# Optimization experiments

Measured on AMD Instinct MI355X. Metric: run time of the kernel, lower is better.

## Reference

```python
import jax, jax.numpy as jnp
import numpy as np

N, D, R, E = 50000, 128, 16, 1600000


def rgcn_conv(x, W, root, bias, src, dst, rel):
    """PyG-style RGCNConv (aggr='mean', root weight + bias).
    out[i] = x[i] @ root + bias + sum_r mean_{j in N_r(i)} x[j] @ W_r
    Aggregate-then-transform: segment-mean per (relation, dst) then contract with W.
    """
    n, d = x.shape
    seg = rel * n + dst  # combined (relation, dst-node) segment id
    msg_sum = jax.ops.segment_sum(x[src], seg, num_segments=R * n).reshape(R, n, d)
    cnt = jax.ops.segment_sum(jnp.ones_like(src, dtype=x.dtype), seg, num_segments=R * n).reshape(R, n, 1)
    msg = msg_sum / jnp.maximum(cnt, 1.0)  # mean aggregation (0 when no edges)
    return jnp.einsum('rnd,rde->ne', msg, W) + x @ root + bias


def setup_inputs() -> dict:
    key = jax.random.key(0)
    ks = jax.random.split(key, 9)
    x = jax.random.normal(ks[0], (N, D), dtype=jnp.float32)
    edge_index = jax.random.randint(ks[1], (2, E), 0, N, dtype=jnp.int64)
    edge_type = jax.random.randint(ks[2], (E,), 0, R, dtype=jnp.int64)
    s = 1.0 / np.sqrt(D)
    W1 = jax.random.normal(ks[3], (R, D, D), dtype=jnp.float32) * s
    root1 = jax.random.normal(ks[4], (D, D), dtype=jnp.float32) * s
    b1 = jnp.zeros((D,), dtype=jnp.float32)
    W2 = jax.random.normal(ks[5], (R, D, D), dtype=jnp.float32) * s
    root2 = jax.random.normal(ks[6], (D, D), dtype=jnp.float32) * s
    b2 = jnp.zeros((D,), dtype=jnp.float32)
    return {"x": x, "edge_index": edge_index, "edge_type": edge_type,
            "W1": W1, "root1": root1, "b1": b1,
            "W2": W2, "root2": root2, "b2": b2}


def reference(x, edge_index, edge_type, W1, root1, b1, W2, root2, b2):
    src, dst = edge_index[0], edge_index[1]
    # layer 1: RGCN -> ReLU -> Dropout (identity in eval mode)
    h = jax.nn.relu(rgcn_conv(x, W1, root1, b1, src, dst, edge_type))
    # layer 2: RGCN -> ReLU
    h = jax.nn.relu(rgcn_conv(h, W2, root2, b2, src, dst, edge_type))
    return h
```

## Files before the change

kernel.cpp:

```cpp
#include <hip/hip_runtime.h>


#define ND 128
#define NR 16
#define KPB 4096

typedef __attribute__((ext_vector_type(8))) short bf16x8;
typedef __attribute__((ext_vector_type(4))) float f32x4;

__device__ __forceinline__ unsigned short f2b(float f) {
    unsigned u = __float_as_uint(f);
    u += 0x7FFFu + ((u >> 16) & 1u);
    return (unsigned short)(u >> 16);
}

__global__ __launch_bounds__(256) void coarse_hist(
    const int* __restrict__ dst, const int* __restrict__ rel,
    int* __restrict__ coarse_cnt, int E, int N, int NBK)
{
    __shared__ int h[1024];
    const int t = threadIdx.x;
    for (int i = t; i < NBK; i += 256) h[i] = 0;
    __syncthreads();
#pragma unroll
    for (int q = 0; q < 16; ++q) {
        int e = blockIdx.x * KPB + q * 256 + t;
        if (e < E) {
            int key = rel[e] * N + dst[e];
            atomicAdd(&h[key >> 12], 1);
        }
    }
    __syncthreads();
    for (int i = t; i < NBK; i += 256)
        if (h[i]) atomicAdd(&coarse_cnt[i], h[i]);
}

__global__ __launch_bounds__(1024) void coarse_scan(
    const int* __restrict__ coarse_cnt, int* __restrict__ cscan,
    int* __restrict__ coarse_cursor, int NBK, int E)
{
    __shared__ int sdata[1024];
    const int t = threadIdx.x;
    int v = (t < NBK) ? coarse_cnt[t] : 0;
    sdata[t] = v;
    __syncthreads();
    for (int off = 1; off < 1024; off <<= 1) {
        int tmp = (t >= off) ? sdata[t - off] : 0;
        __syncthreads();
        sdata[t] += tmp;
        __syncthreads();
    }
    if (t < NBK) {
        int excl = sdata[t] - v;
        cscan[t] = excl;
        coarse_cursor[t] = excl;
    }
    if (t == 0) cscan[NBK] = E;
}

__global__ __launch_bounds__(256) void fillA(
    const int* __restrict__ src, const int* __restrict__ dst,
    const int* __restrict__ rel, int* __restrict__ coarse_cursor,
    uint2* __restrict__ coarse_buf, int E, int N, int NBK)
{
    __shared__ uint2 pairs[KPB];
    __shared__ int h[1024];
    const int t = threadIdx.x;
    for (int i = t; i < NBK; i += 256) h[i] = 0;
    __syncthreads();
#pragma unroll
    for (int q = 0; q < 16; ++q) {
        int e = blockIdx.x * KPB + q * 256 + t;
        unsigned key = 0xFFFFFFFFu, sv = 0;
        if (e < E) {
            key = (unsigned)(rel[e] * N + dst[e]);
            sv = (unsigned)src[e];
            atomicAdd(&h[key >> 12], 1);
        }
        pairs[q * 256 + t] = make_uint2(sv, key);
    }
    __syncthreads();
    for (int i = t; i < NBK; i += 256) {
        int c = h[i];
        h[i] = c ? atomicAdd(&coarse_cursor[i], c) : 0;
    }
    __syncthreads();
#pragma unroll
    for (int q = 0; q < 16; ++q) {
        uint2 p = pairs[q * 256 + t];
        if (p.y != 0xFFFFFFFFu) {
            int pos = atomicAdd(&h[p.y >> 12], 1);
            coarse_buf[pos] = p;
        }
    }
}

__global__ __launch_bounds__(256) void fillB(
    const uint2* __restrict__ coarse_buf, const int* __restrict__ cscan,
    int* __restrict__ seg_off, float* __restrict__ cnt_inv,
    int* __restrict__ sorted_src, int M, int E, int NBK)
{
    __shared__ int cnt[KPB];
    __shared__ int w[256];
    const int t = threadIdx.x;
    const int b = blockIdx.x;
    const int kbase = b << 12;
    const int nkeys = min(KPB, M - kbase);
    const int r0 = cscan[b], r1 = cscan[b + 1];

    for (int i = t; i < KPB; i += 256) cnt[i] = 0;
    __syncthreads();
    for (int e = r0 + t; e < r1; e += 256)
        atomicAdd(&cnt[coarse_buf[e].y - kbase], 1);
    __syncthreads();
    for (int i = t; i < nkeys; i += 256)
        cnt_inv[kbase + i] = 1.0f / fmaxf((float)cnt[i], 1.0f);
    int s = 0;
#pragma unroll
    for (int j = 0; j < 16; ++j) s += cnt[t * 16 + j];
    w[t] = s;
    __syncthreads();
    for (int off = 1; off < 256; off <<= 1) {
        int tmp = (t >= off) ? w[t - off] : 0;
        __syncthreads();
        w[t] += tmp;
        __syncthreads();
    }
    int run = r0 + w[t] - s;
#pragma unroll
    for (int j = 0; j < 16; ++j) {
        int i = t * 16 + j;
        int c = cnt[i];
        cnt[i] = run;
        if (i < nkeys) seg_off[kbase + i] = run;
        run += c;
    }
    if (b == NBK - 1 && t == 0) seg_off[M] = E;
    __syncthreads();
    for (int e = r0 + t; e < r1; e += 256) {
        uint2 p = coarse_buf[e];
        int pos = atomicAdd(&cnt[p.y - kbase], 1);
        sorted_src[pos] = (int)p.x;
    }
}

__global__ __launch_bounds__(256) void conv_x_kernel(
    const float* __restrict__ x, unsigned short* __restrict__ xb, int n4)
{
    int i = blockIdx.x * 256 + threadIdx.x;
    if (i >= n4) return;
    float4 v = ((const float4*)x)[i];
    uint2 o;
    o.x = (unsigned)f2b(v.x) | ((unsigned)f2b(v.y) << 16);
    o.y = (unsigned)f2b(v.z) | ((unsigned)f2b(v.w) << 16);
    ((uint2*)xb)[i] = o;
}

__global__ __launch_bounds__(256) void conv_w_kernel(
    const float* __restrict__ W, const float* __restrict__ root,
    unsigned short* __restrict__ Wt)
{
    int t = blockIdx.x * 256 + threadIdx.x;
    if (t >= 17 * 2048) return;
    int mat = t >> 11;
    int f = t & 2047;
    int lane = f & 63;
    int ctkt = f >> 6;
    int kt = ctkt >> 3;
    int ct = ctkt & 7;
    int n = ct * 16 + (lane & 15);
    int k = kt * 32 + (lane >> 4) * 8;
    const float* s = (mat < 16) ? (W + (size_t)mat * 16384) : root;
    uint4 o;
    o.x = (unsigned)f2b(s[(size_t)(k + 0) * ND + n]) | ((unsigned)f2b(s[(size_t)(k + 1) * ND + n]) << 16);
    o.y = (unsigned)f2b(s[(size_t)(k + 2) * ND + n]) | ((unsigned)f2b(s[(size_t)(k + 3) * ND + n]) << 16);
    o.z = (unsigned)f2b(s[(size_t)(k + 4) * ND + n]) | ((unsigned)f2b(s[(size_t)(k + 5) * ND + n]) << 16);
    o.w = (unsigned)f2b(s[(size_t)(k + 6) * ND + n]) | ((unsigned)f2b(s[(size_t)(k + 7) * ND + n]) << 16);
    *(uint4*)(Wt + (size_t)t * 8) = o;
}

__global__ __launch_bounds__(256) void gather_mean(
    const unsigned short* __restrict__ A,
    const int* __restrict__ seg_off,
    const int* __restrict__ sorted_src,
    const float* __restrict__ cnt_inv,
    unsigned short* __restrict__ msg,
    int N, int r0, int ccN)
{
    int g = blockIdx.x * 16 + (threadIdx.x >> 4);
    if (g >= ccN) return;
    int l = threadIdx.x & 15;
    int s = r0 * N + g;
    int b0 = seg_off[s], e1 = seg_off[s + 1];
    float a0 = 0.f, a1 = 0.f, a2 = 0.f, a3 = 0.f, a4 = 0.f, a5 = 0.f, a6 = 0.f, a7 = 0.f;
    int e = b0;
    for (; e + 2 <= e1; e += 2) {
        int s0 = sorted_src[e];
        int s1 = sorted_src[e + 1];
        uint4 u0 = *(const uint4*)(A + (size_t)s0 * ND + l * 8);
        uint4 u1 = *(const uint4*)(A + (size_t)s1 * ND + l * 8);
        a0 += __uint_as_float(u0.x << 16); a1 += __uint_as_float(u0.x & 0xFFFF0000u);
        a2 += __uint_as_float(u0.y << 16); a3 += __uint_as_float(u0.y & 0xFFFF0000u);
        a4 += __uint_as_float(u0.z << 16); a5 += __uint_as_float(u0.z & 0xFFFF0000u);
        a6 += __uint_as_float(u0.w << 16); a7 += __uint_as_float(u0.w & 0xFFFF0000u);
        a0 += __uint_as_float(u1.x << 16); a1 += __uint_as_float(u1.x & 0xFFFF0000u);
        a2 += __uint_as_float(u1.y << 16); a3 += __uint_as_float(u1.y & 0xFFFF0000u);
        a4 += __uint_as_float(u1.z << 16); a5 += __uint_as_float(u1.z & 0xFFFF0000u);
        a6 += __uint_as_float(u1.w << 16); a7 += __uint_as_float(u1.w & 0xFFFF0000u);
    }
    if (e < e1) {
        int s0 = sorted_src[e];
        uint4 u0 = *(const uint4*)(A + (size_t)s0 * ND + l * 8);
        a0 += __uint_as_float(u0.x << 16); a1 += __uint_as_float(u0.x & 0xFFFF0000u);
        a2 += __uint_as_float(u0.y << 16); a3 += __uint_as_float(u0.y & 0xFFFF0000u);
        a4 += __uint_as_float(u0.z << 16); a5 += __uint_as_float(u0.z & 0xFFFF0000u);
        a6 += __uint_as_float(u0.w << 16); a7 += __uint_as_float(u0.w & 0xFFFF0000u);
    }
    float inv = cnt_inv[s];
    uint4 o;
    o.x = (unsigned)f2b(a0 * inv) | ((unsigned)f2b(a1 * inv) << 16);
    o.y = (unsigned)f2b(a2 * inv) | ((unsigned)f2b(a3 * inv) << 16);
    o.z = (unsigned)f2b(a4 * inv) | ((unsigned)f2b(a5 * inv) << 16);
    o.w = (unsigned)f2b(a6 * inv) | ((unsigned)f2b(a7 * inv) << 16);
    *(uint4*)(msg + (size_t)g * ND + l * 8) = o;
}

__global__ __launch_bounds__(256) void gemm_mfma(
    const unsigned short* __restrict__ msg,
    const unsigned short* __restrict__ xb,
    const unsigned short* __restrict__ Wt,
    const float* __restrict__ bias,
    float* __restrict__ acc_buf,
    unsigned short* __restrict__ out_bf,
    float* __restrict__ out_f32,
    int N, int c0, int cc, int include_root, int load_acc, int finalize)
{
    __shared__ __align__(16) unsigned short Bs[2048 * 8];
    const int tid = threadIdx.x;
    const int lane = tid & 63;
    const int wv = tid >> 6;
    const int quad = lane >> 4;
    const int l16 = lane & 15;
    const int m0 = blockIdx.x * 64 + wv * 16;
    const int arow = m0 + l16;

    f32x4 acc[8];
    if (load_acc) {
#pragma unroll
        for (int ct = 0; ct < 8; ++ct)
#pragma unroll
            for (int rg = 0; rg < 4; ++rg) {
                int r = m0 + quad * 4 + rg;
                acc[ct][rg] = (r < N) ? acc_buf[(size_t)r * ND + ct * 16 + l16] : 0.f;
            }
    } else {
#pragma unroll
        for (int ct = 0; ct < 8; ++ct) { f32x4 z = {0.f, 0.f, 0.f, 0.f}; acc[ct] = z; }
    }

    for (int rel = include_root ? -1 : 0; rel < cc; ++rel) {
        const unsigned short* A = (rel < 0) ? xb : msg + (size_t)rel * N * ND;
        const int mat = (rel < 0) ? 16 : (c0 + rel);
        const uint4* Bsrc = (const uint4*)(Wt + (size_t)mat * 2048 * 8);

        bf16x8 a[4];
#pragma unroll
        for (int kt = 0; kt < 4; ++kt) {
            bf16x8 z = {0, 0, 0, 0, 0, 0, 0, 0};
            a[kt] = (arow < N) ? *(const bf16x8*)(A + (size_t)arow * ND + kt * 32 + quad * 8) : z;
        }

        __syncthreads();
#pragma unroll
        for (int i = 0; i < 8; ++i)
            ((uint4*)Bs)[tid + i * 256] = Bsrc[tid + i * 256];
        __syncthreads();

#pragma unroll
        for (int kt = 0; kt < 4; ++kt) {
#pragma unroll
            for (int ct = 0; ct < 8; ++ct) {
                bf16x8 b = *(const bf16x8*)(Bs + (size_t)((kt * 8 + ct) * 64 + lane) * 8);
                acc[ct] = __builtin_amdgcn_mfma_f32_16x16x32_bf16(a[kt], b, acc[ct], 0, 0, 0);
            }
        }
    }

    if (!finalize) {
#pragma unroll
        for (int ct = 0; ct < 8; ++ct)
#pragma unroll
            for (int rg = 0; rg < 4; ++rg) {
                int r = m0 + quad * 4 + rg;
                if (r < N) acc_buf[(size_t)r * ND + ct * 16 + l16] = acc[ct][rg];
            }
    } else {
#pragma unroll
        for (int ct = 0; ct < 8; ++ct) {
            float bb = bias[ct * 16 + l16];
#pragma unroll
            for (int rg = 0; rg < 4; ++rg) {
                int r = m0 + quad * 4 + rg;
                if (r < N) {
                    float v = fmaxf(acc[ct][rg] + bb, 0.f);
                    if (out_bf) out_bf[(size_t)r * ND + ct * 16 + l16] = f2b(v);
                    else        out_f32[(size_t)r * ND + ct * 16 + l16] = v;
                }
            }
        }
    }
}

extern "C" void kernel_launch(void* const* d_in, const int* in_sizes, int n_in,
                              void* d_out, int out_size, void* d_ws, size_t ws_size,
                              hipStream_t stream) {
    const float* x     = (const float*)d_in[0];
    const int*   eidx  = (const int*)d_in[1];
    const int*   etype = (const int*)d_in[2];
    const float* W1    = (const float*)d_in[3];
    const float* root1 = (const float*)d_in[4];
    const float* b1    = (const float*)d_in[5];
    const float* W2    = (const float*)d_in[6];
    const float* root2 = (const float*)d_in[7];
    const float* b2    = (const float*)d_in[8];
    float* out = (float*)d_out;

    const int N = in_sizes[0] / ND;
    const int E = in_sizes[2];
    const int M = NR * N;
    const int NBK = (M + KPB - 1) / KPB;

    const int* src = eidx;
    const int* dst = eidx + E;

    char* p = (char*)d_ws;
    auto carve = [&](size_t bytes) { char* q = p; p += (bytes + 255) & ~(size_t)255; return q; };
    unsigned short* h_bf    = (unsigned short*)carve((size_t)N * ND * 2);
    unsigned short* x_bf    = (unsigned short*)carve((size_t)N * ND * 2);
    unsigned short* Wt1     = (unsigned short*)carve((size_t)17 * 2048 * 8 * 2);
    unsigned short* Wt2     = (unsigned short*)carve((size_t)17 * 2048 * 8 * 2);
    int*   seg_off          = (int*)  carve((size_t)(M + 1) * 4);
    float* cnt_inv          = (float*)carve((size_t)M * 4);
    int*   sorted_src       = (int*)  carve((size_t)E * 4);
    int*   coarse_cnt       = (int*)  carve(1024 * 4);
    int*   cscan            = (int*)  carve(1025 * 4);
    int*   coarse_cursor    = (int*)  carve(1024 * 4);

    size_t fixed = (size_t)(p - (char*)d_ws);
    size_t remain = (ws_size > fixed) ? ws_size - fixed : 0;
    size_t chunk_bytes = (size_t)N * ND * 2;
    size_t acc_bytes   = (size_t)N * ND * 4;
    int C = 2;
    if (remain >= 16 * chunk_bytes + 512) C = 16;
    else if (remain >= 8 * chunk_bytes + acc_bytes + 512) C = 8;
    else if (remain >= 4 * chunk_bytes + acc_bytes + 512) C = 4;
    uint2* coarse_buf       = (uint2*)p;
    unsigned short* msg     = (unsigned short*)carve((size_t)C * chunk_bytes);
    float* acc              = (float*)((C < 16) ? carve(acc_bytes) : (char*)p);

    const int eb4 = (E + KPB - 1) / KPB;
    const int gemm_blocks = (N + 63) / 64;

    hipMemsetAsync(coarse_cnt, 0, 1024 * 4, stream);
    coarse_hist<<<eb4, 256, 0, stream>>>(dst, etype, coarse_cnt, E, N, NBK);
    coarse_scan<<<1, 1024, 0, stream>>>(coarse_cnt, cscan, coarse_cursor, NBK, E);
    fillA<<<eb4, 256, 0, stream>>>(src, dst, etype, coarse_cursor, coarse_buf, E, N, NBK);
    fillB<<<NBK, 256, 0, stream>>>(coarse_buf, cscan, seg_off, cnt_inv, sorted_src, M, E, NBK);

    conv_x_kernel<<<((N * ND / 4) + 255) / 256, 256, 0, stream>>>(x, x_bf, N * ND / 4);
    conv_w_kernel<<<(17 * 2048 + 255) / 256, 256, 0, stream>>>(W1, root1, Wt1);
    conv_w_kernel<<<(17 * 2048 + 255) / 256, 256, 0, stream>>>(W2, root2, Wt2);

    for (int layer = 0; layer < 2; ++layer) {
        const unsigned short* A  = (layer == 0) ? x_bf : h_bf;
        const unsigned short* Wt = (layer == 0) ? Wt1  : Wt2;
        const float* biasp       = (layer == 0) ? b1   : b2;

        for (int c0 = 0; c0 < NR; c0 += C) {
            int cc = (NR - c0 < C) ? (NR - c0) : C;
            int ccN = cc * N;
            gather_mean<<<(ccN + 15) / 16, 256, 0, stream>>>(
                A, seg_off, sorted_src, cnt_inv, msg, N, c0, ccN);
            int fin = (c0 + cc == NR) ? 1 : 0;
            gemm_mfma<<<gemm_blocks, 256, 0, stream>>>(
                msg, A, Wt, biasp, acc,
                (fin && layer == 0) ? h_bf : (unsigned short*)nullptr,
                (fin && layer == 1) ? out : (float*)nullptr,
                N, c0, cc, c0 == 0 ? 1 : 0, c0 > 0 ? 1 : 0, fin);
        }
    }
}
```

Baseline: 519.1 us.

## Chunk over nodes instead of relations to drop fp32 accumulator round-trips

Work is now split by node chunks rather than relation chunks. Each gather covers all 16 relations for a slice of nodes, and each GEMM block accumulates root plus all relations in registers, then applies bias and ReLU directly. This removes the fp32 accumulator buffer reads and writes between relation chunks, and next-relation A tiles are prefetched while the current B tile loads. The msg buffer now shares space with the coarse sort buffer. When the workspace is small, more node chunks mean more kernel launches and smaller grids.

```diff
diff --git a/kernel.cpp b/kernel.cpp
--- a/kernel.cpp
+++ b/kernel.cpp
@@ -185,12 +185,13 @@
     const int* __restrict__ sorted_src,
     const float* __restrict__ cnt_inv,
     unsigned short* __restrict__ msg,
-    int N, int r0, int ccN)
-{
-    int g = blockIdx.x * 16 + (threadIdx.x >> 4);
-    if (g >= ccN) return;
+    int N, int n0, int nch, int stride)
+{
+    int ln = blockIdx.x * 16 + (threadIdx.x >> 4);
+    if (ln >= nch) return;
+    int r = blockIdx.y;
     int l = threadIdx.x & 15;
-    int s = r0 * N + g;
+    int s = r * N + n0 + ln;
     int b0 = seg_off[s], e1 = seg_off[s + 1];
     float a0 = 0.f, a1 = 0.f, a2 = 0.f, a3 = 0.f, a4 = 0.f, a5 = 0.f, a6 = 0.f, a7 = 0.f;
     int e = b0;
@@ -222,7 +223,7 @@
     o.y = (unsigned)f2b(a2 * inv) | ((unsigned)f2b(a3 * inv) << 16);
     o.z = (unsigned)f2b(a4 * inv) | ((unsigned)f2b(a5 * inv) << 16);
     o.w = (unsigned)f2b(a6 * inv) | ((unsigned)f2b(a7 * inv) << 16);
-    *(uint4*)(msg + (size_t)g * ND + l * 8) = o;
+    *(uint4*)(msg + ((size_t)r * stride + ln) * ND + l * 8) = o;
 }
 
 __global__ __launch_bounds__(256) void gemm_mfma(
@@ -230,10 +231,9 @@
     const unsigned short* __restrict__ xb,
     const unsigned short* __restrict__ Wt,
     const float* __restrict__ bias,
-    float* __restrict__ acc_buf,
     unsigned short* __restrict__ out_bf,
     float* __restrict__ out_f32,
-    int N, int c0, int cc, int include_root, int load_acc, int finalize)
+    int N, int n0, int nch, int stride)
 {
     __shared__ __align__(16) unsigned short Bs[2048 * 8];
     const int tid = threadIdx.x;
@@ -241,39 +241,48 @@
     const int wv = tid >> 6;
     const int quad = lane >> 4;
     const int l16 = lane & 15;
-    const int m0 = blockIdx.x * 64 + wv * 16;
+    const int m0 = n0 + blockIdx.x * 64 + wv * 16;
     const int arow = m0 + l16;
+    const int nend = min(n0 + nch, N);
+    const bool av = (arow < nend);
+    const int lrow = arow - n0;
 
     f32x4 acc[8];
-    if (load_acc) {
-#pragma unroll
-        for (int ct = 0; ct < 8; ++ct)
-#pragma unroll
-            for (int rg = 0; rg < 4; ++rg) {
-                int r = m0 + quad * 4 + rg;
-                acc[ct][rg] = (r < N) ? acc_buf[(size_t)r * ND + ct * 16 + l16] : 0.f;
-            }
+#pragma unroll
+    for (int ct = 0; ct < 8; ++ct) { f32x4 z = {0.f, 0.f, 0.f, 0.f}; acc[ct] = z; }
+
+    bf16x8 a[4];
+    if (av) {
+#pragma unroll
+        for (int kt = 0; kt < 4; ++kt)
+            a[kt] = *(const bf16x8*)(xb + (size_t)arow * ND + kt * 32 + quad * 8);
     } else {
-#pragma unroll
-        for (int ct = 0; ct < 8; ++ct) { f32x4 z = {0.f, 0.f, 0.f, 0.f}; acc[ct] = z; }
-    }
-
-    for (int rel = include_root ? -1 : 0; rel < cc; ++rel) {
-        const unsigned short* A = (rel < 0) ? xb : msg + (size_t)rel * N * ND;
-        const int mat = (rel < 0) ? 16 : (c0 + rel);
+        bf16x8 z = {0, 0, 0, 0, 0, 0, 0, 0};
+#pragma unroll
+        for (int kt = 0; kt < 4; ++kt) a[kt] = z;
+    }
+
+    for (int rel = -1; rel < NR; ++rel) {
+        const int mat = (rel < 0) ? 16 : rel;
         const uint4* Bsrc = (const uint4*)(Wt + (size_t)mat * 2048 * 8);
-
-        bf16x8 a[4];
-#pragma unroll
-        for (int kt = 0; kt < 4; ++kt) {
-            bf16x8 z = {0, 0, 0, 0, 0, 0, 0, 0};
-            a[kt] = (arow < N) ? *(const bf16x8*)(A + (size_t)arow * ND + kt * 32 + quad * 8) : z;
-        }
 
         __syncthreads();
 #pragma unroll
         for (int i = 0; i < 8; ++i)
             ((uint4*)Bs)[tid + i * 256] = Bsrc[tid + i * 256];
+
+        bf16x8 an[4];
+        {
+            bf16x8 z = {0, 0, 0, 0, 0, 0, 0, 0};
+#pragma unroll
+            for (int kt = 0; kt < 4; ++kt) an[kt] = z;
+        }
+        if (rel + 1 < NR && av) {
+            const unsigned short* Ar = msg + ((size_t)(rel + 1) * stride + lrow) * ND + quad * 8;
+#pragma unroll
+            for (int kt = 0; kt < 4; ++kt)
+                an[kt] = *(const bf16x8*)(Ar + kt * 32);
+        }
         __syncthreads();
 
 #pragma unroll
@@ -284,28 +293,20 @@
                 acc[ct] = __builtin_amdgcn_mfma_f32_16x16x32_bf16(a[kt], b, acc[ct], 0, 0, 0);
             }
         }
-    }
-
-    if (!finalize) {
-#pragma unroll
-        for (int ct = 0; ct < 8; ++ct)
-#pragma unroll
-            for (int rg = 0; rg < 4; ++rg) {
-                int r = m0 + quad * 4 + rg;
-                if (r < N) acc_buf[(size_t)r * ND + ct * 16 + l16] = acc[ct][rg];
-            }
-    } else {
-#pragma unroll
-        for (int ct = 0; ct < 8; ++ct) {
-            float bb = bias[ct * 16 + l16];
-#pragma unroll
-            for (int rg = 0; rg < 4; ++rg) {
-                int r = m0 + quad * 4 + rg;
-                if (r < N) {
-                    float v = fmaxf(acc[ct][rg] + bb, 0.f);
-                    if (out_bf) out_bf[(size_t)r * ND + ct * 16 + l16] = f2b(v);
-                    else        out_f32[(size_t)r * ND + ct * 16 + l16] = v;
-                }
+#pragma unroll
+        for (int kt = 0; kt < 4; ++kt) a[kt] = an[kt];
+    }
+
+#pragma unroll
+    for (int ct = 0; ct < 8; ++ct) {
+        float bb = bias[ct * 16 + l16];
+#pragma unroll
+        for (int rg = 0; rg < 4; ++rg) {
+            int r = m0 + quad * 4 + rg;
+            if (r < nend) {
+                float v = fmaxf(acc[ct][rg] + bb, 0.f);
+                if (out_bf) out_bf[(size_t)r * ND + ct * 16 + l16] = f2b(v);
+                else        out_f32[(size_t)r * ND + ct * 16 + l16] = v;
             }
         }
     }
@@ -348,20 +349,21 @@
 
     size_t fixed = (size_t)(p - (char*)d_ws);
     size_t remain = (ws_size > fixed) ? ws_size - fixed : 0;
-    size_t chunk_bytes = (size_t)N * ND * 2;
-    size_t acc_bytes   = (size_t)N * ND * 4;
-    int C = 2;
-    if (remain >= 16 * chunk_bytes + 512) C = 16;
-    else if (remain >= 8 * chunk_bytes + acc_bytes + 512) C = 8;
-    else if (remain >= 4 * chunk_bytes + acc_bytes + 512) C = 4;
+    int NCH = 2, chunk;
+    size_t msg_bytes;
+    while (true) {
+        chunk = (((N + NCH - 1) / NCH) + 63) & ~63;
+        msg_bytes = (size_t)NR * chunk * ND * 2;
+        if (msg_bytes + 512 <= remain || NCH >= 16) break;
+        NCH *= 2;
+    }
+    size_t union_bytes = msg_bytes > (size_t)E * 8 ? msg_bytes : (size_t)E * 8;
     uint2* coarse_buf       = (uint2*)p;
-    unsigned short* msg     = (unsigned short*)carve((size_t)C * chunk_bytes);
-    float* acc              = (float*)((C < 16) ? carve(acc_bytes) : (char*)p);
+    unsigned short* msg     = (unsigned short*)carve(union_bytes);
 
     const int eb4 = (E + KPB - 1) / KPB;
-    const int gemm_blocks = (N + 63) / 64;
-
-    hipMemsetAsync(coarse_cnt, 0, 1024 * 4, stream);
+
+    (void)hipMemsetAsync(coarse_cnt, 0, 1024 * 4, stream);
     coarse_hist<<<eb4, 256, 0, stream>>>(dst, etype, coarse_cnt, E, N, NBK);
     coarse_scan<<<1, 1024, 0, stream>>>(coarse_cnt, cscan, coarse_cursor, NBK, E);
     fillA<<<eb4, 256, 0, stream>>>(src, dst, etype, coarse_cursor, coarse_buf, E, N, NBK);
@@ -376,17 +378,15 @@
         const unsigned short* Wt = (layer == 0) ? Wt1  : Wt2;
         const float* biasp       = (layer == 0) ? b1   : b2;
 
-        for (int c0 = 0; c0 < NR; c0 += C) {
-            int cc = (NR - c0 < C) ? (NR - c0) : C;
-            int ccN = cc * N;
-            gather_mean<<<(ccN + 15) / 16, 256, 0, stream>>>(
-                A, seg_off, sorted_src, cnt_inv, msg, N, c0, ccN);
-            int fin = (c0 + cc == NR) ? 1 : 0;
-            gemm_mfma<<<gemm_blocks, 256, 0, stream>>>(
-                msg, A, Wt, biasp, acc,
-                (fin && layer == 0) ? h_bf : (unsigned short*)nullptr,
-                (fin && layer == 1) ? out : (float*)nullptr,
-                N, c0, cc, c0 == 0 ? 1 : 0, c0 > 0 ? 1 : 0, fin);
-        }
-    }
-}
+        for (int n0 = 0; n0 < N; n0 += chunk) {
+            int nch = (N - n0 < chunk) ? (N - n0) : chunk;
+            gather_mean<<<dim3((nch + 15) / 16, NR), 256, 0, stream>>>(
+                A, seg_off, sorted_src, cnt_inv, msg, N, n0, nch, chunk);
+            gemm_mfma<<<(nch + 63) / 64, 256, 0, stream>>>(
+                msg, A, Wt, biasp,
+                (layer == 0) ? h_bf : (unsigned short*)nullptr,
+                (layer == 1) ? out : (float*)nullptr,
+                N, n0, nch, chunk);
+        }
+    }
+}
```

Result: slower. 589.5 us (+13.6%).

## Reorder RGCN to transform-then-aggregate with per-node multi-relation accumulation

Applied to the files above, without the earlier changes.

Computes x@W_r for chunks of four relations (plus root in the last chunk) into bf16 buffers, then gathers transformed rows per destination node and accumulates means across relations, fusing bias and ReLU at the end. This removes the materialized per-relation mean messages and the fp32 GEMM accumulator round-trips. In exchange it adds more kernel launches and an intermediate accumulator kept in bf16 between chunks, which reduces precision.

```diff
diff --git a/kernel.cpp b/kernel.cpp
--- a/kernel.cpp
+++ b/kernel.cpp
@@ -179,61 +179,11 @@
     *(uint4*)(Wt + (size_t)t * 8) = o;
 }
 
-__global__ __launch_bounds__(256) void gather_mean(
+__global__ __launch_bounds__(256) void gemm_y(
     const unsigned short* __restrict__ A,
-    const int* __restrict__ seg_off,
-    const int* __restrict__ sorted_src,
-    const float* __restrict__ cnt_inv,
-    unsigned short* __restrict__ msg,
-    int N, int r0, int ccN)
-{
-    int g = blockIdx.x * 16 + (threadIdx.x >> 4);
-    if (g >= ccN) return;
-    int l = threadIdx.x & 15;
-    int s = r0 * N + g;
-    int b0 = seg_off[s], e1 = seg_off[s + 1];
-    float a0 = 0.f, a1 = 0.f, a2 = 0.f, a3 = 0.f, a4 = 0.f, a5 = 0.f, a6 = 0.f, a7 = 0.f;
-    int e = b0;
-    for (; e + 2 <= e1; e += 2) {
-        int s0 = sorted_src[e];
-        int s1 = sorted_src[e + 1];
-        uint4 u0 = *(const uint4*)(A + (size_t)s0 * ND + l * 8);
-        uint4 u1 = *(const uint4*)(A + (size_t)s1 * ND + l * 8);
-        a0 += __uint_as_float(u0.x << 16); a1 += __uint_as_float(u0.x & 0xFFFF0000u);
-        a2 += __uint_as_float(u0.y << 16); a3 += __uint_as_float(u0.y & 0xFFFF0000u);
-        a4 += __uint_as_float(u0.z << 16); a5 += __uint_as_float(u0.z & 0xFFFF0000u);
-        a6 += __uint_as_float(u0.w << 16); a7 += __uint_as_float(u0.w & 0xFFFF0000u);
-        a0 += __uint_as_float(u1.x << 16); a1 += __uint_as_float(u1.x & 0xFFFF0000u);
-        a2 += __uint_as_float(u1.y << 16); a3 += __uint_as_float(u1.y & 0xFFFF0000u);
-        a4 += __uint_as_float(u1.z << 16); a5 += __uint_as_float(u1.z & 0xFFFF0000u);
-        a6 += __uint_as_float(u1.w << 16); a7 += __uint_as_float(u1.w & 0xFFFF0000u);
-    }
-    if (e < e1) {
-        int s0 = sorted_src[e];
-        uint4 u0 = *(const uint4*)(A + (size_t)s0 * ND + l * 8);
-        a0 += __uint_as_float(u0.x << 16); a1 += __uint_as_float(u0.x & 0xFFFF0000u);
-        a2 += __uint_as_float(u0.y << 16); a3 += __uint_as_float(u0.y & 0xFFFF0000u);
-        a4 += __uint_as_float(u0.z << 16); a5 += __uint_as_float(u0.z & 0xFFFF0000u);
-        a6 += __uint_as_float(u0.w << 16); a7 += __uint_as_float(u0.w & 0xFFFF0000u);
-    }
-    float inv = cnt_inv[s];
-    uint4 o;
-    o.x = (unsigned)f2b(a0 * inv) | ((unsigned)f2b(a1 * inv) << 16);
-    o.y = (unsigned)f2b(a2 * inv) | ((unsigned)f2b(a3 * inv) << 16);
-    o.z = (unsigned)f2b(a4 * inv) | ((unsigned)f2b(a5 * inv) << 16);
-    o.w = (unsigned)f2b(a6 * inv) | ((unsigned)f2b(a7 * inv) << 16);
-    *(uint4*)(msg + (size_t)g * ND + l * 8) = o;
-}
-
-__global__ __launch_bounds__(256) void gemm_mfma(
-    const unsigned short* __restrict__ msg,
-    const unsigned short* __restrict__ xb,
     const unsigned short* __restrict__ Wt,
-    const float* __restrict__ bias,
-    float* __restrict__ acc_buf,
-    unsigned short* __restrict__ out_bf,
-    float* __restrict__ out_f32,
-    int N, int c0, int cc, int include_root, int load_acc, int finalize)
+    unsigned short* __restrict__ Y,
+    int N, int c0, int nmats, int inc_root)
 {
     __shared__ __align__(16) unsigned short Bs[2048 * 8];
     const int tid = threadIdx.x;
@@ -244,31 +194,20 @@
     const int m0 = blockIdx.x * 64 + wv * 16;
     const int arow = m0 + l16;
 
-    f32x4 acc[8];
-    if (load_acc) {
-#pragma unroll
-        for (int ct = 0; ct < 8; ++ct)
-#pragma unroll
-            for (int rg = 0; rg < 4; ++rg) {
-                int r = m0 + quad * 4 + rg;
-                acc[ct][rg] = (r < N) ? acc_buf[(size_t)r * ND + ct * 16 + l16] : 0.f;
-            }
+    bf16x8 a[4];
+    if (arow < N) {
+#pragma unroll
+        for (int kt = 0; kt < 4; ++kt)
+            a[kt] = *(const bf16x8*)(A + (size_t)arow * ND + kt * 32 + quad * 8);
     } else {
-#pragma unroll
-        for (int ct = 0; ct < 8; ++ct) { f32x4 z = {0.f, 0.f, 0.f, 0.f}; acc[ct] = z; }
-    }
-
-    for (int rel = include_root ? -1 : 0; rel < cc; ++rel) {
-        const unsigned short* A = (rel < 0) ? xb : msg + (size_t)rel * N * ND;
-        const int mat = (rel < 0) ? 16 : (c0 + rel);
+        bf16x8 z = {0, 0, 0, 0, 0, 0, 0, 0};
+#pragma unroll
+        for (int kt = 0; kt < 4; ++kt) a[kt] = z;
+    }
+
+    for (int m = 0; m < nmats; ++m) {
+        const int mat = (inc_root && m == nmats - 1) ? 16 : (c0 + m);
         const uint4* Bsrc = (const uint4*)(Wt + (size_t)mat * 2048 * 8);
-
-        bf16x8 a[4];
-#pragma unroll
-        for (int kt = 0; kt < 4; ++kt) {
-            bf16x8 z = {0, 0, 0, 0, 0, 0, 0, 0};
-            a[kt] = (arow < N) ? *(const bf16x8*)(A + (size_t)arow * ND + kt * 32 + quad * 8) : z;
-        }
 
         __syncthreads();
 #pragma unroll
@@ -276,6 +215,9 @@
             ((uint4*)Bs)[tid + i * 256] = Bsrc[tid + i * 256];
         __syncthreads();
 
+        f32x4 acc[8];
+#pragma unroll
+        for (int ct = 0; ct < 8; ++ct) { f32x4 z = {0.f, 0.f, 0.f, 0.f}; acc[ct] = z; }
 #pragma unroll
         for (int kt = 0; kt < 4; ++kt) {
 #pragma unroll
@@ -284,29 +226,106 @@
                 acc[ct] = __builtin_amdgcn_mfma_f32_16x16x32_bf16(a[kt], b, acc[ct], 0, 0, 0);
             }
         }
-    }
-
-    if (!finalize) {
+
+        unsigned short* Ym = Y + (size_t)m * N * ND;
 #pragma unroll
         for (int ct = 0; ct < 8; ++ct)
 #pragma unroll
             for (int rg = 0; rg < 4; ++rg) {
                 int r = m0 + quad * 4 + rg;
-                if (r < N) acc_buf[(size_t)r * ND + ct * 16 + l16] = acc[ct][rg];
+                if (r < N) Ym[(size_t)r * ND + ct * 16 + l16] = f2b(acc[ct][rg]);
             }
+    }
+}
+
+__global__ __launch_bounds__(256) void aggregate(
+    const unsigned short* __restrict__ Y,
+    const int* __restrict__ seg_off,
+    const int* __restrict__ sorted_src,
+    const float* __restrict__ cnt_inv,
+    unsigned short* __restrict__ accb,
+    const float* __restrict__ bias,
+    unsigned short* __restrict__ out_bf,
+    float* __restrict__ out_f32,
+    int N, int c0, int cc, int first, int last, int root_slot)
+{
+    int d = blockIdx.x * 16 + (threadIdx.x >> 4);
+    if (d >= N) return;
+    int l = threadIdx.x & 15;
+    float t0 = 0.f, t1 = 0.f, t2 = 0.f, t3 = 0.f, t4 = 0.f, t5 = 0.f, t6 = 0.f, t7 = 0.f;
+
+    for (int rc = 0; rc < cc; ++rc) {
+        int s = (c0 + rc) * N + d;
+        int b0 = seg_off[s], e1 = seg_off[s + 1];
+        if (b0 == e1) continue;
+        const unsigned short* Yr = Y + (size_t)rc * N * ND;
+        float a0 = 0.f, a1 = 0.f, a2 = 0.f, a3 = 0.f, a4 = 0.f, a5 = 0.f, a6 = 0.f, a7 = 0.f;
+        int e = b0;
+        for (; e + 2 <= e1; e += 2) {
+            int s0 = sorted_src[e];
+            int s1 = sorted_src[e + 1];
+            uint4 u0 = *(const uint4*)(Yr + (size_t)s0 * ND + l * 8);
+            uint4 u1 = *(const uint4*)(Yr + (size_t)s1 * ND + l * 8);
+            a0 += __uint_as_float(u0.x << 16); a1 += __uint_as_float(u0.x & 0xFFFF0000u);
+            a2 += __uint_as_float(u0.y << 16); a3 += __uint_as_float(u0.y & 0xFFFF0000u);
+            a4 += __uint_as_float(u0.z << 16); a5 += __uint_as_float(u0.z & 0xFFFF0000u);
+            a6 += __uint_as_float(u0.w << 16); a7 += __uint_as_float(u0.w & 0xFFFF0000u);
+            a0 += __uint_as_float(u1.x << 16); a1 += __uint_as_float(u1.x & 0xFFFF0000u);
+            a2 += __uint_as_float(u1.y << 16); a3 += __uint_as_float(u1.y & 0xFFFF0000u);
+            a4 += __uint_as_float(u1.z << 16); a5 += __uint_as_float(u1.z & 0xFFFF0000u);
+            a6 += __uint_as_float(u1.w << 16); a7 += __uint_as_float(u1.w & 0xFFFF0000u);
+        }
+        if (e < e1) {
+            int s0 = sorted_src[e];
+            uint4 u0 = *(const uint4*)(Yr + (size_t)s0 * ND + l * 8);
+            a0 += __uint_as_float(u0.x << 16); a1 += __uint_as_float(u0.x & 0xFFFF0000u);
+            a2 += __uint_as_float(u0.y << 16); a3 += __uint_as_float(u0.y & 0xFFFF0000u);
+            a4 += __uint_as_float(u0.z << 16); a5 += __uint_as_float(u0.z & 0xFFFF0000u);
+            a6 += __uint_as_float(u0.w << 16); a7 += __uint_as_float(u0.w & 0xFFFF0000u);
+        }
+        float inv = cnt_inv[s];
+        t0 += inv * a0; t1 += inv * a1; t2 += inv * a2; t3 += inv * a3;
+        t4 += inv * a4; t5 += inv * a5; t6 += inv * a6; t7 += inv * a7;
+    }
+
+    if (!first) {
+        uint4 u = *(const uint4*)(accb + (size_t)d * ND + l * 8);
+        t0 += __uint_as_float(u.x << 16); t1 += __uint_as_float(u.x & 0xFFFF0000u);
+        t2 += __uint_as_float(u.y << 16); t3 += __uint_as_float(u.y & 0xFFFF0000u);
+        t4 += __uint_as_float(u.z << 16); t5 += __uint_as_float(u.z & 0xFFFF0000u);
+        t6 += __uint_as_float(u.w << 16); t7 += __uint_as_float(u.w & 0xFFFF0000u);
+    }
+
+    if (!last) {
+        uint4 o;
+        o.x = (unsigned)f2b(t0) | ((unsigned)f2b(t1) << 16);
+        o.y = (unsigned)f2b(t2) | ((unsigned)f2b(t3) << 16);
+        o.z = (unsigned)f2b(t4) | ((unsigned)f2b(t5) << 16);
+        o.w = (unsigned)f2b(t6) | ((unsigned)f2b(t7) << 16);
+        *(uint4*)(accb + (size_t)d * ND + l * 8) = o;
     } else {
-#pragma unroll
-        for (int ct = 0; ct < 8; ++ct) {
-            float bb = bias[ct * 16 + l16];
-#pragma unroll
-            for (int rg = 0; rg < 4; ++rg) {
-                int r = m0 + quad * 4 + rg;
-                if (r < N) {
-                    float v = fmaxf(acc[ct][rg] + bb, 0.f);
-                    if (out_bf) out_bf[(size_t)r * ND + ct * 16 + l16] = f2b(v);
-                    else        out_f32[(size_t)r * ND + ct * 16 + l16] = v;
-                }
-            }
+        uint4 u = *(const uint4*)(Y + ((size_t)root_slot * N + d) * ND + l * 8);
+        t0 += __uint_as_float(u.x << 16); t1 += __uint_as_float(u.x & 0xFFFF0000u);
+        t2 += __uint_as_float(u.y << 16); t3 += __uint_as_float(u.y & 0xFFFF0000u);
+        t4 += __uint_as_float(u.z << 16); t5 += __uint_as_float(u.z & 0xFFFF0000u);
+        t6 += __uint_as_float(u.w << 16); t7 += __uint_as_float(u.w & 0xFFFF0000u);
+        float4 b0 = ((const float4*)bias)[l * 2];
+        float4 b1 = ((const float4*)bias)[l * 2 + 1];
+        t0 = fmaxf(t0 + b0.x, 0.f); t1 = fmaxf(t1 + b0.y, 0.f);
+        t2 = fmaxf(t2 + b0.z, 0.f); t3 = fmaxf(t3 + b0.w, 0.f);
+        t4 = fmaxf(t4 + b1.x, 0.f); t5 = fmaxf(t5 + b1.y, 0.f);
+        t6 = fmaxf(t6 + b1.z, 0.f); t7 = fmaxf(t7 + b1.w, 0.f);
+        if (out_bf) {
+            uint4 o;
+            o.x = (unsigned)f2b(t0) | ((unsigned)f2b(t1) << 16);
+            o.y = (unsigned)f2b(t2) | ((unsigned)f2b(t3) << 16);
+            o.z = (unsigned)f2b(t4) | ((unsigned)f2b(t5) << 16);
+            o.w = (unsigned)f2b(t6) | ((unsigned)f2b(t7) << 16);
+            *(uint4*)(out_bf + (size_t)d * ND + l * 8) = o;
+        } else {
+            float4* op = (float4*)(out_f32 + (size_t)d * ND);
+            op[l * 2]     = make_float4(t0, t1, t2, t3);
+            op[l * 2 + 1] = make_float4(t4, t5, t6, t7);
         }
     }
 }
@@ -345,23 +364,18 @@
     int*   coarse_cnt       = (int*)  carve(1024 * 4);
     int*   cscan            = (int*)  carve(1025 * 4);
     int*   coarse_cursor    = (int*)  carve(1024 * 4);
-
-    size_t fixed = (size_t)(p - (char*)d_ws);
-    size_t remain = (ws_size > fixed) ? ws_size - fixed : 0;
-    size_t chunk_bytes = (size_t)N * ND * 2;
-    size_t acc_bytes   = (size_t)N * ND * 4;
-    int C = 2;
-    if (remain >= 16 * chunk_bytes + 512) C = 16;
-    else if (remain >= 8 * chunk_bytes + acc_bytes + 512) C = 8;
-    else if (remain >= 4 * chunk_bytes + acc_bytes + 512) C = 4;
+    unsigned short* accb    = (unsigned short*)carve((size_t)N * ND * 2);
+
+    size_t y_bytes = (size_t)5 * N * ND * 2;
+    size_t union_bytes = y_bytes > (size_t)E * 8 ? y_bytes : (size_t)E * 8;
     uint2* coarse_buf       = (uint2*)p;
-    unsigned short* msg     = (unsigned short*)carve((size_t)C * chunk_bytes);
-    float* acc              = (float*)((C < 16) ? carve(acc_bytes) : (char*)p);
+    unsigned short* Y       = (unsigned short*)carve(union_bytes);
 
     const int eb4 = (E + KPB - 1) / KPB;
     const int gemm_blocks = (N + 63) / 64;
-
-    hipMemsetAsync(coarse_cnt, 0, 1024 * 4, stream);
+    const int agg_blocks  = (N + 15) / 16;
+
+    (void)hipMemsetAsync(coarse_cnt, 0, 1024 * 4, stream);
     coarse_hist<<<eb4, 256, 0, stream>>>(dst, etype, coarse_cnt, E, N, NBK);
     coarse_scan<<<1, 1024, 0, stream>>>(coarse_cnt, cscan, coarse_cursor, NBK, E);
     fillA<<<eb4, 256, 0, stream>>>(src, dst, etype, coarse_cursor, coarse_buf, E, N, NBK);
@@ -376,17 +390,16 @@
         const unsigned short* Wt = (layer == 0) ? Wt1  : Wt2;
         const float* biasp       = (layer == 0) ? b1   : b2;
 
-        for (int c0 = 0; c0 < NR; c0 += C) {
-            int cc = (NR - c0 < C) ? (NR - c0) : C;
-            int ccN = cc * N;
-            gather_mean<<<(ccN + 15) / 16, 256, 0, stream>>>(
-                A, seg_off, sorted_src, cnt_inv, msg, N, c0, ccN);
-            int fin = (c0 + cc == NR) ? 1 : 0;
-            gemm_mfma<<<gemm_blocks, 256, 0, stream>>>(
-                msg, A, Wt, biasp, acc,
-                (fin && layer == 0) ? h_bf : (unsigned short*)nullptr,
-                (fin && layer == 1) ? out : (float*)nullptr,
-                N, c0, cc, c0 == 0 ? 1 : 0, c0 > 0 ? 1 : 0, fin);
-        }
-    }
-}
+        for (int ci = 0; ci < 4; ++ci) {
+            int c0 = ci * 4;
+            int inc_root = (ci == 3) ? 1 : 0;
+            int nmats = 4 + inc_root;
+            gemm_y<<<gemm_blocks, 256, 0, stream>>>(A, Wt, Y, N, c0, nmats, inc_root);
+            aggregate<<<agg_blocks, 256, 0, stream>>>(
+                Y, seg_off, sorted_src, cnt_inv, accb, biasp,
+                (inc_root && layer == 0) ? h_bf : (unsigned short*)nullptr,
+                (inc_root && layer == 1) ? out : (float*)nullptr,
+                N, c0, 4, ci == 0 ? 1 : 0, inc_root, 4);
+        }
+    }
+}
```

After: 598.1 us. 1.15x slower.
